# Optimization experiments

Hardware: AMD Instinct MI355X
Metric: run time of the kernel (lower is better)

## Reference

```python
import jax, jax.numpy as jnp
import numpy as np

TOP_K = 2
CAPACITY_FACTOR = 1.0


def _ffn(x, w1, w2):
    # SwiGLU FFN: x [N, D], w1 [D, 2F], w2 [F, D]
    h = x @ w1
    x1, x2 = jnp.split(h, 2, axis=-1)
    return (x1 * jax.nn.silu(x2)) @ w2


def setup_inputs() -> dict:
    key = jax.random.key(0)
    ks = jax.random.split(key, 6)
    B, S, D, F, E_r, E_s = 4, 2048, 2048, 1024, 7, 1
    sc_in = 1.0 / np.sqrt(D)
    sc_mid = 1.0 / np.sqrt(F)
    return {
        "x": jax.random.normal(ks[0], (B, S, D), dtype=jnp.float32),
        "gate_w": jax.random.normal(ks[1], (D, E_r), dtype=jnp.float32) * sc_in,
        "expert_bias": jnp.zeros((E_r,), dtype=jnp.float32),
        "shared_w1": jax.random.normal(ks[2], (E_s, D, 2 * F), dtype=jnp.float32) * sc_in,
        "shared_w2": jax.random.normal(ks[3], (E_s, F, D), dtype=jnp.float32) * sc_mid,
        "routed_w1": jax.random.normal(ks[4], (E_r, D, 2 * F), dtype=jnp.float32) * sc_in,
        "routed_w2": jax.random.normal(ks[5], (E_r, F, D), dtype=jnp.float32) * sc_mid,
    }


def reference(x, gate_w, expert_bias, shared_w1, shared_w2, routed_w1, routed_w2):
    B, S, D = x.shape
    E_r = gate_w.shape[1]
    T = B * S
    capacity = max(1, int(CAPACITY_FACTOR * T / E_r))
    flat_x = x.reshape(T, D)

    # shared experts: applied to every token, summed
    shared_sum = jax.vmap(_ffn, in_axes=(None, 0, 0))(flat_x, shared_w1, shared_w2).sum(0)

    # gating (eval mode: no noise, no dropout)
    gate_logits = flat_x @ gate_w + expert_bias  # [T, E_r]
    aff = jax.nn.sigmoid(gate_logits)
    _, topk_idx = jax.lax.top_k(aff, TOP_K)  # [T, K]
    # mask[t, e] = expert e is among token t's top-k
    mask = (topk_idx[:, :, None] == jnp.arange(E_r)[None, None, :]).any(axis=1)  # [T, E_r]

    # per-expert capacity selection: keep top-`capacity` masked tokens by affinity
    score = jnp.where(mask, aff, -1.0).T  # [E_r, T]; aff >= 0 so -1 sorts last
    _, sel_idx = jax.lax.top_k(score, capacity)  # [E_r, capacity] token ids
    kept = jnp.take_along_axis(mask.T, sel_idx, axis=1)  # [E_r, cap]
    w = jnp.where(kept, jnp.take_along_axis(aff.T, sel_idx, axis=1), 0.0)  # [E_r, cap]

    # grouped gather -> FFN -> weighted scatter-add
    inp = flat_x[sel_idx]  # [E_r, cap, D]
    out = jax.vmap(_ffn)(inp, routed_w1, routed_w2)  # [E_r, cap, D]
    routed_sum = jnp.zeros_like(flat_x).at[sel_idx].add(out * w[:, :, None])

    return (shared_sum + routed_sum).reshape(B, S, D)
```

## Files before the change

### kernel.cpp

```cpp
#include <hip/hip_runtime.h>
#include <hip/hip_bf16.h>

typedef unsigned long long u64;
typedef __bf16 bf16x8 __attribute__((ext_vector_type(8)));
typedef float f32x4 __attribute__((ext_vector_type(4)));
typedef unsigned short ushort8_t __attribute__((ext_vector_type(8)));

#define TOKS 8192
#define DMODEL 2048
#define FD 1024
#define NEXP 7
#define CAP 1170
#define CAPP 1280
#define URT256 67

#define MFMA16(a, b, c) __builtin_amdgcn_mfma_f32_16x16x32_bf16(a, b, c, 0, 0, 0)

__device__ __forceinline__ unsigned short f2bf(float f) {
  __hip_bfloat16 b = __float2bfloat16(f);
  return __builtin_bit_cast(unsigned short, b);
}
__device__ __forceinline__ float bf2f(unsigned short u) {
  __hip_bfloat16 b = __builtin_bit_cast(__hip_bfloat16, u);
  return __bfloat162float(b);
}
__device__ __forceinline__ void gload_lds16(const void* g, void* l) {
  __builtin_amdgcn_global_load_lds(
      (const __attribute__((address_space(1))) void*)g,
      (__attribute__((address_space(3))) void*)l, 16, 0, 0);
}

__global__ __launch_bounds__(256) void k_conv_gate(
    const float* __restrict__ x, const float* __restrict__ gw,
    const float* __restrict__ bias, unsigned short* __restrict__ xb,
    u64* __restrict__ keys) {
  const int t = blockIdx.x;
  const int tid = threadIdx.x;
  const int lane = tid & 63, wv = tid >> 6;
  const float* xr = x + (long)t * DMODEL;
  const int i0 = tid * 8;
  float4 v0 = *(const float4*)&xr[i0];
  float4 v1 = *(const float4*)&xr[i0 + 4];
  float xv[8] = {v0.x, v0.y, v0.z, v0.w, v1.x, v1.y, v1.z, v1.w};
  ushort8_t o;
#pragma unroll
  for (int j = 0; j < 8; ++j) o[j] = f2bf(xv[j]);
  *(ushort8_t*)&xb[(long)t * DMODEL + i0] = o;
  double acc[NEXP];
#pragma unroll
  for (int e = 0; e < NEXP; ++e) acc[e] = 0.0;
#pragma unroll
  for (int j = 0; j < 8; ++j) {
    const float* g = gw + (long)(i0 + j) * NEXP;
    double xd = (double)xv[j];
#pragma unroll
    for (int e = 0; e < NEXP; ++e) acc[e] += xd * (double)g[e];
  }
#pragma unroll
  for (int e = 0; e < NEXP; ++e)
    for (int off = 32; off > 0; off >>= 1)
      acc[e] += __shfl_down(acc[e], off, 64);
  __shared__ double red[4][NEXP];
  if (lane == 0)
#pragma unroll
    for (int e = 0; e < NEXP; ++e) red[wv][e] = acc[e];
  __syncthreads();
  if (tid == 0) {
    float aff[NEXP];
#pragma unroll
    for (int e = 0; e < NEXP; ++e) {
      double lg = red[0][e] + red[1][e] + red[2][e] + red[3][e] + (double)bias[e];
      aff[e] = (float)(1.0 / (1.0 + exp(-lg)));
    }
    int i1 = 0;
    for (int e = 1; e < NEXP; ++e) if (aff[e] > aff[i1]) i1 = e;
    int i2 = -1;
    for (int e = 0; e < NEXP; ++e) {
      if (e == i1) continue;
      if (i2 < 0 || aff[e] > aff[i2]) i2 = e;
    }
#pragma unroll
    for (int e = 0; e < NEXP; ++e) {
      u64 key = (u64)(0xFFFFFFFFu - (unsigned)t);
      if (e == i1 || e == i2) key |= ((u64)__float_as_uint(aff[e])) << 32;
      keys[(long)e * TOKS + t] = key;
    }
  }
}

template <bool PERM>
__global__ void k_transpose_bf16(const float* __restrict__ in0,
                                 const float* __restrict__ inr,
                                 unsigned short* __restrict__ out,
                                 int R, int C) {
  __shared__ float tile[32][33];
  int z = blockIdx.z;
  const float* in = (z == 0) ? in0 : (inr + (long)(z - 1) * R * C);
  unsigned short* o = out + (long)z * R * C;
  int c0 = blockIdx.x * 32;
  int r0 = blockIdx.y * 32;
  int tx = threadIdx.x, ty = threadIdx.y;
#pragma unroll
  for (int k = 0; k < 4; ++k)
    tile[ty + 8 * k][tx] = in[(long)(r0 + ty + 8 * k) * C + c0 + tx];
  __syncthreads();
#pragma unroll
  for (int k = 0; k < 4; ++k) {
    int c = c0 + ty + 8 * k;
    long orow = PERM ? (long)(((c & 1023) >> 4) * 32 + ((c >> 10) << 4) + (c & 15))
                     : (long)c;
    o[orow * R + r0 + tx] = f2bf(tile[tx][ty + 8 * k]);
  }
}

__global__ __launch_bounds__(1024) void k_select(
    const u64* __restrict__ keys, int* __restrict__ sel,
    float* __restrict__ selw, unsigned* __restrict__ cnt,
    int* __restrict__ inv) {
  __shared__ unsigned hist[256];
  __shared__ u64 s_prefix;
  __shared__ unsigned s_k;
  __shared__ unsigned s_cnt;
  const int e = blockIdx.x;
  const u64* kk = keys + (long)e * TOKS;
  const int tid = threadIdx.x;
  if (tid == 0) { s_prefix = 0; s_k = CAP; s_cnt = 0; }
  __syncthreads();
  for (int shift = 56; shift >= 0; shift -= 8) {
    if (tid < 256) hist[tid] = 0;
    __syncthreads();
    u64 pref = s_prefix;
    for (int i = tid; i < TOKS; i += 1024) {
      u64 key = kk[i];
      bool match = (shift == 56) || ((key >> (shift + 8)) == pref);
      if (match) atomicAdd(&hist[(unsigned)(key >> shift) & 255u], 1u);
    }
    __syncthreads();
    if (tid == 0) {
      unsigned k = s_k, cum = 0;
      for (int b = 255; b >= 0; --b) {
        unsigned c = hist[b];
        if (cum + c >= k) {
          s_prefix = (s_prefix << 8) | (unsigned)b;
          s_k = k - cum;
          break;
        }
        cum += c;
      }
    }
    __syncthreads();
  }
  const u64 T = s_prefix;
  for (int i = tid; i < TOKS; i += 1024) {
    u64 key = kk[i];
    if (key >= T) {
      unsigned p = atomicAdd(&s_cnt, 1u);
      int tok = (int)(0xFFFFFFFFu - (unsigned)(key & 0xFFFFFFFFull));
      unsigned vb = (unsigned)(key >> 32);
      sel[e * CAPP + p] = tok;
      selw[e * CAPP + p] = vb ? __uint_as_float(vb) : 0.0f;
      if (vb) {
        unsigned pos = atomicAdd(&cnt[tok], 1u);
        inv[tok * 2 + pos] = e * CAPP + (int)p;
      }
    }
  }
  for (int i = CAP + tid; i < CAPP; i += 1024) {
    sel[e * CAPP + i] = 0;
    selw[e * CAPP + i] = 0.0f;
  }
}

__global__ __launch_bounds__(256) void k_combine(
    float* __restrict__ out, const unsigned short* __restrict__ rout,
    const int* __restrict__ inv, const unsigned* __restrict__ cnt) {
  const int tok = blockIdx.x;
  const unsigned c = cnt[tok];
  if (c == 0) return;
  int i0 = inv[tok * 2];
  int i1 = (c > 1) ? inv[tok * 2 + 1] : -1;
  if (c > 1 && i1 < i0) { int t = i0; i0 = i1; i1 = t; }
  const int col = threadIdx.x * 8;
  float* o = out + (long)tok * DMODEL + col;
  float4 v0 = *(float4*)o;
  float4 v1 = *(float4*)(o + 4);
  ushort8_t r0 = *(const ushort8_t*)&rout[(long)i0 * DMODEL + col];
  v0.x += bf2f(r0[0]); v0.y += bf2f(r0[1]); v0.z += bf2f(r0[2]); v0.w += bf2f(r0[3]);
  v1.x += bf2f(r0[4]); v1.y += bf2f(r0[5]); v1.z += bf2f(r0[6]); v1.w += bf2f(r0[7]);
  if (c > 1) {
    ushort8_t r1 = *(const ushort8_t*)&rout[(long)i1 * DMODEL + col];
    v0.x += bf2f(r1[0]); v0.y += bf2f(r1[1]); v0.z += bf2f(r1[2]); v0.w += bf2f(r1[3]);
    v1.x += bf2f(r1[4]); v1.y += bf2f(r1[5]); v1.z += bf2f(r1[6]); v1.w += bf2f(r1[7]);
  }
  *(float4*)o = v0;
  *(float4*)(o + 4) = v1;
}

template <int WHICH>
__global__ __launch_bounds__(512, 2) void k_ffn8(
    const unsigned short* __restrict__ Abase,
    const unsigned short* __restrict__ Wbase,
    unsigned short* __restrict__ a_all, float* __restrict__ out,
    unsigned short* __restrict__ r_out,
    const int* __restrict__ sel, const float* __restrict__ selw) {
  constexpr int K = (WHICH == 1) ? DMODEL : FD;
  constexpr int N = 2048;
  constexpr int nk = K >> 6;
  extern __shared__ unsigned short lds[];
  const int tid = threadIdx.x;
  const int w = tid >> 6;
  const int lane = tid & 63;

  const int bx = blockIdx.x;
  const int by_u = blockIdx.y;

  int e, zw, m0l;
  if (by_u < 32) { e = -1; zw = 0; m0l = by_u << 8; }
  else { int q = by_u - 32; e = q / 5; zw = e + 1; m0l = (q % 5) << 8; }
  const long crow0_u = (e < 0) ? (long)m0l : (8192 + (long)e * CAPP + m0l);
  const long n0 = (long)bx * 256;
  const unsigned short* Bm = Wbase + (long)zw * N * K;

  const int wr = w >> 2;
  const int wc = w & 3;
  const int lr = lane & 15;
  const int kq = lane >> 4;

  const unsigned short* aP[2][2];
  const unsigned short* bP[2][2];
  int dstOff[2];
#pragma unroll
  for (int j = 0; j < 2; ++j) {
    int L = w * 128 + j * 64 + lane;
    int r = L >> 3;
    int cEl = ((L & 7) * 8) ^ ((r & 7) * 8);
    dstOff[j] = (w * 2 + j) * 512;
#pragma unroll
    for (int h = 0; h < 2; ++h) {
      long ar;
      if (WHICH == 1)
        ar = (e < 0) ? (long)(m0l + h * 128 + r)
                     : (long)sel[e * CAPP + m0l + h * 128 + r];
      else
        ar = crow0_u + h * 128 + r;
      aP[h][j] = Abase + ar * (long)K + cEl;
      bP[h][j] = Bm + (n0 + h * 128 + r) * (long)K + cEl;
    }
  }

  auto STAGE = [&](int seg, int d, int ts) {
    unsigned short* base = lds + ((d << 2) + seg) * 8192;
    const unsigned short *p0, *p1;
    if (seg < 2) { p0 = aP[seg][0]; p1 = aP[seg][1]; }
    else         { p0 = bP[seg - 2][0]; p1 = bP[seg - 2][1]; }
    long ko = (long)ts * 64;
    gload_lds16(p0 + ko, base + dstOff[0]);
    gload_lds16(p1 + ko, base + dstOff[1]);
  };

  const int aSegT = wr;
  const int bSegT = 2 + (wc >> 1);
  const int colSw0 = (kq * 8) ^ ((lr & 7) * 8);
  const int colSw1 = (32 + kq * 8) ^ ((lr & 7) * 8);
  const int bRow = (wc & 1) * 64 + lr;

  STAGE(0, 0, 0); STAGE(1, 0, 0); STAGE(2, 0, 0); STAGE(3, 0, 0);
  if (nk > 1) { STAGE(0, 1, 1); STAGE(1, 1, 1); }
  else        { STAGE(0, 1, 0); STAGE(1, 1, 0); }
  asm volatile("s_waitcnt vmcnt(4)" ::: "memory");
  __builtin_amdgcn_sched_barrier(0);
  __builtin_amdgcn_s_barrier();
  __builtin_amdgcn_sched_barrier(0);

  f32x4 acc[8][4] = {};

#pragma unroll 1
  for (int T = 0; T < nk; ++T) {
    const int d = T & 1, dn = d ^ 1;
    int t1 = T + 1; if (t1 >= nk) t1 -= nk;
    int t2 = T + 2; if (t2 >= nk) t2 -= nk;
    const unsigned short* aSeg = lds + ((d << 2) + aSegT) * 8192;
    const unsigned short* bSeg = lds + ((d << 2) + bSegT) * 8192;
    bf16x8 af[8], b0, b1;

#pragma unroll
    for (int m = 0; m < 8; ++m)
      af[m] = *(const bf16x8*)&aSeg[(m * 16 + lr) * 64 + colSw0];
    b0 = *(const bf16x8*)&bSeg[(bRow + 0) * 64 + colSw0];
    b1 = *(const bf16x8*)&bSeg[(bRow + 16) * 64 + colSw0];
    __builtin_amdgcn_sched_barrier(0);
    STAGE(2, dn, t1);
    __builtin_amdgcn_sched_barrier(0);
    __builtin_amdgcn_s_barrier();
    asm volatile("s_waitcnt lgkmcnt(0)" ::: "memory");
    __builtin_amdgcn_sched_barrier(0);
    __builtin_amdgcn_s_setprio(1);
#pragma unroll
    for (int m = 0; m < 8; ++m) {
      acc[m][0] = MFMA16(af[m], b0, acc[m][0]);
      acc[m][1] = MFMA16(af[m], b1, acc[m][1]);
    }
    __builtin_amdgcn_s_setprio(0);
    __builtin_amdgcn_sched_barrier(0);
    __builtin_amdgcn_s_barrier();
    __builtin_amdgcn_sched_barrier(0);

    b0 = *(const bf16x8*)&bSeg[(bRow + 32) * 64 + colSw0];
    b1 = *(const bf16x8*)&bSeg[(bRow + 48) * 64 + colSw0];
    __builtin_amdgcn_sched_barrier(0);
    STAGE(3, dn, t1);
    __builtin_amdgcn_sched_barrier(0);
    __builtin_amdgcn_s_barrier();
    asm volatile("s_waitcnt lgkmcnt(0)" ::: "memory");
    __builtin_amdgcn_sched_barrier(0);
    __builtin_amdgcn_s_setprio(1);
#pragma unroll
    for (int m = 0; m < 8; ++m) {
      acc[m][2] = MFMA16(af[m], b0, acc[m][2]);
      acc[m][3] = MFMA16(af[m], b1, acc[m][3]);
    }
    __builtin_amdgcn_s_setprio(0);
    __builtin_amdgcn_sched_barrier(0);
    __builtin_amdgcn_s_barrier();
    __builtin_amdgcn_sched_barrier(0);

#pragma unroll
    for (int m = 0; m < 8; ++m)
      af[m] = *(const bf16x8*)&aSeg[(m * 16 + lr) * 64 + colSw1];
    b0 = *(const bf16x8*)&bSeg[(bRow + 0) * 64 + colSw1];
    b1 = *(const bf16x8*)&bSeg[(bRow + 16) * 64 + colSw1];
    __builtin_amdgcn_sched_barrier(0);
    __builtin_amdgcn_s_barrier();
    asm volatile("s_waitcnt lgkmcnt(0)" ::: "memory");
    __builtin_amdgcn_sched_barrier(0);
    __builtin_amdgcn_s_setprio(1);
#pragma unroll
    for (int m = 0; m < 8; ++m) {
      acc[m][0] = MFMA16(af[m], b0, acc[m][0]);
      acc[m][1] = MFMA16(af[m], b1, acc[m][1]);
    }
    __builtin_amdgcn_s_setprio(0);
    __builtin_amdgcn_sched_barrier(0);
    __builtin_amdgcn_s_barrier();
    __builtin_amdgcn_sched_barrier(0);

    b0 = *(const bf16x8*)&bSeg[(bRow + 32) * 64 + colSw1];
    b1 = *(const bf16x8*)&bSeg[(bRow + 48) * 64 + colSw1];
    __builtin_amdgcn_sched_barrier(0);
    STAGE(0, d, t2);
    STAGE(1, d, t2);
    asm volatile("s_waitcnt vmcnt(4)" ::: "memory");
    __builtin_amdgcn_sched_barrier(0);
    __builtin_amdgcn_s_barrier();
    asm volatile("s_waitcnt lgkmcnt(0)" ::: "memory");
    __builtin_amdgcn_sched_barrier(0);
    __builtin_amdgcn_s_setprio(1);
#pragma unroll
    for (int m = 0; m < 8; ++m) {
      acc[m][2] = MFMA16(af[m], b0, acc[m][2]);
      acc[m][3] = MFMA16(af[m], b1, acc[m][3]);
    }
    __builtin_amdgcn_s_setprio(0);
    __builtin_amdgcn_sched_barrier(0);
    __builtin_amdgcn_s_barrier();
    __builtin_amdgcn_sched_barrier(0);
  }
  asm volatile("s_waitcnt vmcnt(0)" ::: "memory");

  const int r0q = (lane >> 4) * 4;
  const int cc = lane & 15;

  if (WHICH == 1) {
    const long gcol0 = (n0 >> 1) + wc * 32;
#pragma unroll
    for (int m = 0; m < 8; ++m)
#pragma unroll
      for (int rj = 0; rj < 4; ++rj) {
        long row = crow0_u + wr * 128 + m * 16 + r0q + rj;
#pragma unroll
        for (int q2 = 0; q2 < 2; ++q2) {
          float x1v = acc[m][2 * q2][rj];
          float x2v = acc[m][2 * q2 + 1][rj];
          float s = x2v / (1.0f + __expf(-x2v));
          a_all[row * FD + gcol0 + q2 * 16 + cc] = f2bf(x1v * s);
        }
      }
  } else {
    const long ccol0 = n0 + wc * 64;
    if (e < 0) {
#pragma unroll
      for (int m = 0; m < 8; ++m)
#pragma unroll
        for (int rj = 0; rj < 4; ++rj) {
          long row = m0l + wr * 128 + m * 16 + r0q + rj;
#pragma unroll
          for (int n = 0; n < 4; ++n)
            out[row * DMODEL + ccol0 + n * 16 + cc] = acc[m][n][rj];
        }
    } else {
#pragma unroll
      for (int m = 0; m < 8; ++m)
#pragma unroll
        for (int rj = 0; rj < 4; ++rj) {
          int lrow = m0l + wr * 128 + m * 16 + r0q + rj;
          float wgt = selw[e * CAPP + lrow];
          unsigned short* C = r_out + ((long)e * CAPP + lrow) * DMODEL;
#pragma unroll
          for (int n = 0; n < 4; ++n)
            C[ccol0 + n * 16 + cc] = f2bf(acc[m][n][rj] * wgt);
        }
    }
  }
}

extern "C" void kernel_launch(void* const* d_in, const int* in_sizes, int n_in,
                              void* d_out, int out_size, void* d_ws,
                              size_t ws_size, hipStream_t stream) {
  (void)in_sizes; (void)n_in; (void)out_size; (void)ws_size;
  const float* x = (const float*)d_in[0];
  const float* gw = (const float*)d_in[1];
  const float* eb = (const float*)d_in[2];
  const float* sw1 = (const float*)d_in[3];
  const float* sw2 = (const float*)d_in[4];
  const float* rw1 = (const float*)d_in[5];
  const float* rw2 = (const float*)d_in[6];
  float* out = (float*)d_out;

  char* ws = (char*)d_ws;
  size_t off = 0;
  auto alloc = [&](size_t bytes) {
    size_t o = off;
    off += (bytes + 255) & ~(size_t)255;
    return o;
  };
  unsigned short* xb    = (unsigned short*)(ws + alloc((size_t)TOKS * DMODEL * 2));
  unsigned short* w1t   = (unsigned short*)(ws + alloc((size_t)8 * DMODEL * (2 * FD) * 2));
  unsigned short* w2t   = (unsigned short*)(ws + alloc((size_t)8 * DMODEL * FD * 2));
  unsigned short* a_all = (unsigned short*)(ws + alloc((size_t)(TOKS + NEXP * CAPP) * FD * 2));
  unsigned short* r_out = (unsigned short*)(ws + alloc((size_t)NEXP * CAPP * DMODEL * 2));
  u64* keys = (u64*)(ws + alloc((size_t)NEXP * TOKS * 8));
  int* sel  = (int*)(ws + alloc((size_t)NEXP * CAPP * 4));
  float* selw = (float*)(ws + alloc((size_t)NEXP * CAPP * 4));
  unsigned* cnt = (unsigned*)(ws + alloc((size_t)TOKS * 4));
  int* inv = (int*)(ws + alloc((size_t)TOKS * 2 * 4));

  const size_t LDSB = 131072;

  k_conv_gate<<<TOKS, 256, 0, stream>>>(x, gw, eb, xb, keys);
  dim3 tb(32, 8);
  k_transpose_bf16<true><<<dim3(64, 64, 8), tb, 0, stream>>>(sw1, rw1, w1t, DMODEL, 2 * FD);
  k_transpose_bf16<false><<<dim3(64, 32, 8), tb, 0, stream>>>(sw2, rw2, w2t, FD, DMODEL);
  hipMemsetAsync(cnt, 0, (size_t)TOKS * 4, stream);
  k_select<<<NEXP, 1024, 0, stream>>>(keys, sel, selw, cnt, inv);
  k_ffn8<1><<<dim3(8, URT256), 512, LDSB, stream>>>(xb, w1t, a_all, nullptr,
                                                    nullptr, sel, nullptr);
  k_ffn8<2><<<dim3(8, URT256), 512, LDSB, stream>>>(a_all, w2t, nullptr, out,
                                                    r_out, nullptr, selw);
  k_combine<<<TOKS, 256, 0, stream>>>(out, r_out, inv, cnt);
}
```

Before: 504.3 us.

## Split FFN kernels, retile second GEMM to 128x128 with grouped scheduling

The second GEMM gets its own kernel using 128x128 tiles with a 32-wide K step, double-buffered LDS and a remapped block order that groups tiles for L2 reuse. It writes bf16 output for both shared and routed rows into one buffer, and the combine kernel now sums the shared and routed rows into the fp32 output. The weight transpose now uses 64x64 tiles with float4 loads and 16-byte stores. The aim is better occupancy and load balance for the K=1024 GEMM and fewer small memory transactions in the transpose. In exchange the shared-expert output is rounded to bf16 and an extra intermediate buffer must be written and read back.

```diff
diff --git a/kernel.cpp b/kernel.cpp
--- a/kernel.cpp
+++ b/kernel.cpp
@@ -13,6 +13,7 @@
 #define CAP 1170
 #define CAPP 1280
 #define URT256 67
+#define URT128 134
 
 #define MFMA16(a, b, c) __builtin_amdgcn_mfma_f32_16x16x32_bf16(a, b, c, 0, 0, 0)
 
@@ -89,27 +90,40 @@
 }
 
 template <bool PERM>
-__global__ void k_transpose_bf16(const float* __restrict__ in0,
-                                 const float* __restrict__ inr,
-                                 unsigned short* __restrict__ out,
-                                 int R, int C) {
-  __shared__ float tile[32][33];
-  int z = blockIdx.z;
+__global__ __launch_bounds__(256) void k_tr64(
+    const float* __restrict__ in0, const float* __restrict__ inr,
+    unsigned short* __restrict__ out, int R, int C) {
+  __shared__ float t[64][65];
+  const int z = blockIdx.z;
   const float* in = (z == 0) ? in0 : (inr + (long)(z - 1) * R * C);
   unsigned short* o = out + (long)z * R * C;
-  int c0 = blockIdx.x * 32;
-  int r0 = blockIdx.y * 32;
-  int tx = threadIdx.x, ty = threadIdx.y;
-#pragma unroll
-  for (int k = 0; k < 4; ++k)
-    tile[ty + 8 * k][tx] = in[(long)(r0 + ty + 8 * k) * C + c0 + tx];
+  const int c0 = blockIdx.x * 64;
+  const int r0 = blockIdx.y * 64;
+  const int tid = threadIdx.x;
+  const int rr = tid >> 4;
+  const int cc4 = (tid & 15) * 4;
+#pragma unroll
+  for (int i = 0; i < 4; ++i) {
+    int r = rr + 16 * i;
+    float4 v = *(const float4*)&in[(long)(r0 + r) * C + c0 + cc4];
+    t[r][cc4 + 0] = v.x;
+    t[r][cc4 + 1] = v.y;
+    t[r][cc4 + 2] = v.z;
+    t[r][cc4 + 3] = v.w;
+  }
   __syncthreads();
 #pragma unroll
-  for (int k = 0; k < 4; ++k) {
-    int c = c0 + ty + 8 * k;
-    long orow = PERM ? (long)(((c & 1023) >> 4) * 32 + ((c >> 10) << 4) + (c & 15))
-                     : (long)c;
-    o[orow * R + r0 + tx] = f2bf(tile[tx][ty + 8 * k]);
+  for (int h = 0; h < 2; ++h) {
+    int c = tid + h * 256;
+    int oc = c >> 3;
+    int j = c & 7;
+    ushort8_t v8;
+#pragma unroll
+    for (int q = 0; q < 8; ++q) v8[q] = f2bf(t[j * 8 + q][oc]);
+    int gc = c0 + oc;
+    long orow = PERM ? (long)(((gc & 1023) >> 4) * 32 + ((gc >> 10) << 4) + (gc & 15))
+                     : (long)gc;
+    *(ushort8_t*)&o[orow * R + r0 + j * 8] = v8;
   }
 }
 
@@ -172,38 +186,43 @@
 }
 
 __global__ __launch_bounds__(256) void k_combine(
-    float* __restrict__ out, const unsigned short* __restrict__ rout,
+    float* __restrict__ out, const unsigned short* __restrict__ o_all,
     const int* __restrict__ inv, const unsigned* __restrict__ cnt) {
   const int tok = blockIdx.x;
   const unsigned c = cnt[tok];
-  if (c == 0) return;
-  int i0 = inv[tok * 2];
-  int i1 = (c > 1) ? inv[tok * 2 + 1] : -1;
-  if (c > 1 && i1 < i0) { int t = i0; i0 = i1; i1 = t; }
+  int i0 = -1, i1 = -1;
+  if (c > 0) {
+    i0 = inv[tok * 2];
+    if (c > 1) {
+      i1 = inv[tok * 2 + 1];
+      if (i1 < i0) { int t = i0; i0 = i1; i1 = t; }
+    }
+  }
   const int col = threadIdx.x * 8;
-  float* o = out + (long)tok * DMODEL + col;
-  float4 v0 = *(float4*)o;
-  float4 v1 = *(float4*)(o + 4);
-  ushort8_t r0 = *(const ushort8_t*)&rout[(long)i0 * DMODEL + col];
-  v0.x += bf2f(r0[0]); v0.y += bf2f(r0[1]); v0.z += bf2f(r0[2]); v0.w += bf2f(r0[3]);
-  v1.x += bf2f(r0[4]); v1.y += bf2f(r0[5]); v1.z += bf2f(r0[6]); v1.w += bf2f(r0[7]);
-  if (c > 1) {
-    ushort8_t r1 = *(const ushort8_t*)&rout[(long)i1 * DMODEL + col];
-    v0.x += bf2f(r1[0]); v0.y += bf2f(r1[1]); v0.z += bf2f(r1[2]); v0.w += bf2f(r1[3]);
-    v1.x += bf2f(r1[4]); v1.y += bf2f(r1[5]); v1.z += bf2f(r1[6]); v1.w += bf2f(r1[7]);
-  }
-  *(float4*)o = v0;
-  *(float4*)(o + 4) = v1;
-}
-
-template <int WHICH>
-__global__ __launch_bounds__(512, 2) void k_ffn8(
+  ushort8_t s = *(const ushort8_t*)&o_all[(long)tok * DMODEL + col];
+  float v[8];
+#pragma unroll
+  for (int q = 0; q < 8; ++q) v[q] = bf2f(s[q]);
+  if (i0 >= 0) {
+    ushort8_t r = *(const ushort8_t*)&o_all[(long)(TOKS + i0) * DMODEL + col];
+#pragma unroll
+    for (int q = 0; q < 8; ++q) v[q] += bf2f(r[q]);
+  }
+  if (i1 >= 0) {
+    ushort8_t r = *(const ushort8_t*)&o_all[(long)(TOKS + i1) * DMODEL + col];
+#pragma unroll
+    for (int q = 0; q < 8; ++q) v[q] += bf2f(r[q]);
+  }
+  float* op = out + (long)tok * DMODEL + col;
+  *(float4*)op = make_float4(v[0], v[1], v[2], v[3]);
+  *(float4*)(op + 4) = make_float4(v[4], v[5], v[6], v[7]);
+}
+
+__global__ __launch_bounds__(512, 2) void k_g1(
     const unsigned short* __restrict__ Abase,
     const unsigned short* __restrict__ Wbase,
-    unsigned short* __restrict__ a_all, float* __restrict__ out,
-    unsigned short* __restrict__ r_out,
-    const int* __restrict__ sel, const float* __restrict__ selw) {
-  constexpr int K = (WHICH == 1) ? DMODEL : FD;
+    unsigned short* __restrict__ a_all, const int* __restrict__ sel) {
+  constexpr int K = DMODEL;
   constexpr int N = 2048;
   constexpr int nk = K >> 6;
   extern __shared__ unsigned short lds[];
@@ -237,12 +256,8 @@
     dstOff[j] = (w * 2 + j) * 512;
 #pragma unroll
     for (int h = 0; h < 2; ++h) {
-      long ar;
-      if (WHICH == 1)
-        ar = (e < 0) ? (long)(m0l + h * 128 + r)
-                     : (long)sel[e * CAPP + m0l + h * 128 + r];
-      else
-        ar = crow0_u + h * 128 + r;
+      long ar = (e < 0) ? (long)(m0l + h * 128 + r)
+                        : (long)sel[e * CAPP + m0l + h * 128 + r];
       aP[h][j] = Abase + ar * (long)K + cEl;
       bP[h][j] = Bm + (n0 + h * 128 + r) * (long)K + cEl;
     }
@@ -265,8 +280,7 @@
   const int bRow = (wc & 1) * 64 + lr;
 
   STAGE(0, 0, 0); STAGE(1, 0, 0); STAGE(2, 0, 0); STAGE(3, 0, 0);
-  if (nk > 1) { STAGE(0, 1, 1); STAGE(1, 1, 1); }
-  else        { STAGE(0, 1, 0); STAGE(1, 1, 0); }
+  STAGE(0, 1, 1); STAGE(1, 1, 1);
   asm volatile("s_waitcnt vmcnt(4)" ::: "memory");
   __builtin_amdgcn_sched_barrier(0);
   __builtin_amdgcn_s_barrier();
@@ -369,48 +383,130 @@
 
   const int r0q = (lane >> 4) * 4;
   const int cc = lane & 15;
-
-  if (WHICH == 1) {
-    const long gcol0 = (n0 >> 1) + wc * 32;
-#pragma unroll
-    for (int m = 0; m < 8; ++m)
-#pragma unroll
-      for (int rj = 0; rj < 4; ++rj) {
-        long row = crow0_u + wr * 128 + m * 16 + r0q + rj;
-#pragma unroll
-        for (int q2 = 0; q2 < 2; ++q2) {
-          float x1v = acc[m][2 * q2][rj];
-          float x2v = acc[m][2 * q2 + 1][rj];
-          float s = x2v / (1.0f + __expf(-x2v));
-          a_all[row * FD + gcol0 + q2 * 16 + cc] = f2bf(x1v * s);
-        }
+  const long gcol0 = (n0 >> 1) + wc * 32;
+#pragma unroll
+  for (int m = 0; m < 8; ++m)
+#pragma unroll
+    for (int rj = 0; rj < 4; ++rj) {
+      long row = crow0_u + wr * 128 + m * 16 + r0q + rj;
+#pragma unroll
+      for (int q2 = 0; q2 < 2; ++q2) {
+        float x1v = acc[m][2 * q2][rj];
+        float x2v = acc[m][2 * q2 + 1][rj];
+        float s = x2v / (1.0f + __expf(-x2v));
+        a_all[row * FD + gcol0 + q2 * 16 + cc] = f2bf(x1v * s);
       }
-  } else {
-    const long ccol0 = n0 + wc * 64;
-    if (e < 0) {
-#pragma unroll
-      for (int m = 0; m < 8; ++m)
-#pragma unroll
-        for (int rj = 0; rj < 4; ++rj) {
-          long row = m0l + wr * 128 + m * 16 + r0q + rj;
-#pragma unroll
-          for (int n = 0; n < 4; ++n)
-            out[row * DMODEL + ccol0 + n * 16 + cc] = acc[m][n][rj];
-        }
-    } else {
-#pragma unroll
-      for (int m = 0; m < 8; ++m)
-#pragma unroll
-        for (int rj = 0; rj < 4; ++rj) {
-          int lrow = m0l + wr * 128 + m * 16 + r0q + rj;
-          float wgt = selw[e * CAPP + lrow];
-          unsigned short* C = r_out + ((long)e * CAPP + lrow) * DMODEL;
-#pragma unroll
-          for (int n = 0; n < 4; ++n)
-            C[ccol0 + n * 16 + cc] = f2bf(acc[m][n][rj] * wgt);
-        }
-    }
-  }
+    }
+}
+
+__global__ __launch_bounds__(512, 4) void k_g2(
+    const unsigned short* __restrict__ Abase,
+    const unsigned short* __restrict__ Wbase,
+    unsigned short* __restrict__ o_all, const float* __restrict__ selw) {
+  constexpr int K = FD;
+  constexpr int N = DMODEL;
+  constexpr int nk = K >> 5;
+  __shared__ unsigned short lds[2][8192];
+  const int tid = threadIdx.x & 255;
+  const int isUpper = 0;
+  (void)isUpper;
+  const int w = tid >> 6;
+  const int lane = tid & 63;
+
+  int lin = blockIdx.x + ((int)blockIdx.y << 4);
+  int gt = (lin & 7) * 268 + (lin >> 3);
+  int ct, rt, su;
+  if (gt < 2048) { su = gt >> 7; int rr = gt & 127; ct = rr >> 3; rt = rr & 7; }
+  else           { su = 16;      int rr = gt - 2048; ct = rr / 6; rt = rr % 6; }
+  const int by_u = su * 8 + rt;
+  const int bx = ct;
+
+  int e, zw, m0l;
+  if (by_u < 64) { e = -1; zw = 0; m0l = by_u << 7; }
+  else { int q = by_u - 64; e = q / 10; zw = e + 1; m0l = (q % 10) << 7; }
+  const long crow0_u = (e < 0) ? (long)m0l : (8192 + (long)e * CAPP + m0l);
+  const long n0 = (long)bx * 128;
+  const unsigned short* Bm = Wbase + (long)zw * N * K;
+
+  const int r_ = (w << 4) + (lane >> 2);
+  const int p_ = lane & 3;
+  const unsigned short* aSrc[2];
+  const unsigned short* bSrc[2];
+#pragma unroll
+  for (int c = 0; c < 2; ++c) {
+    int rsg = c * 64 + r_;
+    int q = p_ ^ ((rsg >> 1) & 3);
+    aSrc[c] = Abase + (crow0_u + rsg) * (long)K + q * 8;
+    bSrc[c] = Bm + (n0 + rsg) * (long)K + q * 8;
+  }
+  const int dst0 = tid * 8;
+
+  auto STAGE = [&](int buf, int kt) {
+    const long ko = (long)kt * 32;
+#pragma unroll
+    for (int c = 0; c < 2; ++c) {
+      gload_lds16(aSrc[c] + ko, &lds[buf][c * 2048 + dst0]);
+      gload_lds16(bSrc[c] + ko, &lds[buf][4096 + c * 2048 + dst0]);
+    }
+  };
+
+  const int wr = w >> 1, wc = w & 1;
+  const int lr = lane & 15, kq = lane >> 4;
+  const int slot = (kq ^ ((lr >> 1) & 3)) * 8;
+  const int aRow = wr * 64 + lr;
+  const int bRow = wc * 64 + lr;
+
+  STAGE(0, 0);
+  asm volatile("s_waitcnt vmcnt(0)" ::: "memory");
+  __builtin_amdgcn_sched_barrier(0);
+  __builtin_amdgcn_s_barrier();
+  __builtin_amdgcn_sched_barrier(0);
+
+  f32x4 acc[4][4] = {};
+  int cur = 0;
+
+#pragma unroll 1
+  for (int kt = 0; kt < nk; ++kt) {
+    if (kt + 1 < nk) STAGE(cur ^ 1, kt + 1);
+    const unsigned short* aSeg = &lds[cur][0];
+    const unsigned short* bSeg = &lds[cur][4096];
+    bf16x8 af[4], bf[4];
+#pragma unroll
+    for (int m = 0; m < 4; ++m)
+      af[m] = *(const bf16x8*)&aSeg[(aRow + m * 16) * 32 + slot];
+#pragma unroll
+    for (int n = 0; n < 4; ++n)
+      bf[n] = *(const bf16x8*)&bSeg[(bRow + n * 16) * 32 + slot];
+    asm volatile("s_waitcnt lgkmcnt(0)" ::: "memory");
+    __builtin_amdgcn_sched_barrier(0);
+    __builtin_amdgcn_s_setprio(1);
+#pragma unroll
+    for (int m = 0; m < 4; ++m)
+#pragma unroll
+      for (int n = 0; n < 4; ++n)
+        acc[m][n] = MFMA16(af[m], bf[n], acc[m][n]);
+    __builtin_amdgcn_s_setprio(0);
+    asm volatile("s_waitcnt vmcnt(0)" ::: "memory");
+    __builtin_amdgcn_sched_barrier(0);
+    __builtin_amdgcn_s_barrier();
+    __builtin_amdgcn_sched_barrier(0);
+    cur ^= 1;
+  }
+
+  const int r0q = (lane >> 4) * 4;
+  const int cc = lane & 15;
+  const long ccol0 = n0 + wc * 64;
+#pragma unroll
+  for (int m = 0; m < 4; ++m)
+#pragma unroll
+    for (int rj = 0; rj < 4; ++rj) {
+      int lrow = m0l + wr * 64 + m * 16 + r0q + rj;
+      float wgt = (e < 0) ? 1.0f : selw[e * CAPP + (lrow - m0l) + (m0l)];
+      long row = crow0_u + wr * 64 + m * 16 + r0q + rj;
+#pragma unroll
+      for (int n = 0; n < 4; ++n)
+        o_all[row * DMODEL + ccol0 + n * 16 + cc] = f2bf(acc[m][n][rj] * wgt);
+    }
 }
 
 extern "C" void kernel_launch(void* const* d_in, const int* in_sizes, int n_in,
@@ -437,7 +533,7 @@
   unsigned short* w1t   = (unsigned short*)(ws + alloc((size_t)8 * DMODEL * (2 * FD) * 2));
   unsigned short* w2t   = (unsigned short*)(ws + alloc((size_t)8 * DMODEL * FD * 2));
   unsigned short* a_all = (unsigned short*)(ws + alloc((size_t)(TOKS + NEXP * CAPP) * FD * 2));
-  unsigned short* r_out = (unsigned short*)(ws + alloc((size_t)NEXP * CAPP * DMODEL * 2));
+  unsigned short* o_all = (unsigned short*)(ws + alloc((size_t)(TOKS + NEXP * CAPP) * DMODEL * 2));
   u64* keys = (u64*)(ws + alloc((size_t)NEXP * TOKS * 8));
   int* sel  = (int*)(ws + alloc((size_t)NEXP * CAPP * 4));
   float* selw = (float*)(ws + alloc((size_t)NEXP * CAPP * 4));
@@ -447,14 +543,11 @@
   const size_t LDSB = 131072;
 
   k_conv_gate<<<TOKS, 256, 0, stream>>>(x, gw, eb, xb, keys);
-  dim3 tb(32, 8);
-  k_transpose_bf16<true><<<dim3(64, 64, 8), tb, 0, stream>>>(sw1, rw1, w1t, DMODEL, 2 * FD);
-  k_transpose_bf16<false><<<dim3(64, 32, 8), tb, 0, stream>>>(sw2, rw2, w2t, FD, DMODEL);
+  k_tr64<true><<<dim3(32, 32, 8), 256, 0, stream>>>(sw1, rw1, w1t, DMODEL, 2 * FD);
+  k_tr64<false><<<dim3(32, 16, 8), 256, 0, stream>>>(sw2, rw2, w2t, FD, DMODEL);
   hipMemsetAsync(cnt, 0, (size_t)TOKS * 4, stream);
   k_select<<<NEXP, 1024, 0, stream>>>(keys, sel, selw, cnt, inv);
-  k_ffn8<1><<<dim3(8, URT256), 512, LDSB, stream>>>(xb, w1t, a_all, nullptr,
-                                                    nullptr, sel, nullptr);
-  k_ffn8<2><<<dim3(8, URT256), 512, LDSB, stream>>>(a_all, w2t, nullptr, out,
-                                                    r_out, nullptr, selw);
-  k_combine<<<TOKS, 256, 0, stream>>>(out, r_out, inv, cnt);
-}
+  k_g1<<<dim3(8, URT256), 512, LDSB, stream>>>(xb, w1t, a_all, sel);
+  k_g2<<<dim3(16, URT128), 256, 0, stream>>>(a_all, w2t, o_all, selw);
+  k_combine<<<TOKS, 256, 0, stream>>>(out, o_all, inv, cnt);
+}
```

New measurement: 496.5 us. No clear change (-1.6%).
